# Kernel optimization log

Measured on AMD Instinct MI355X. Metric: run time of the kernel, lower is better.

## Reference

```python
import jax, jax.numpy as jnp
import numpy as np

N = 100000
E = 2000000
IN_DIM = 5
D = 32
L = 3
EPS = 1e-5


def setup_inputs() -> dict:
    key = jax.random.key(0)
    ks = jax.random.split(key, 10)
    x = jax.random.normal(ks[0], (N, IN_DIM), dtype=jnp.float32)
    edge_index = jax.random.randint(ks[1], (2, E), 0, N, dtype=jnp.int64)
    s = 1.0 / np.sqrt(D)
    w_in = jax.random.normal(ks[2], (D, IN_DIM), dtype=jnp.float32) / np.sqrt(IN_DIM)
    b_in = jnp.zeros((D,), dtype=jnp.float32)
    w_l = jax.random.normal(ks[3], (L, D, D), dtype=jnp.float32) * s  # lin_l per layer
    b_l = jnp.zeros((L, D), dtype=jnp.float32)
    w_r = jax.random.normal(ks[4], (L, D, D), dtype=jnp.float32) * s  # lin_r per layer (no bias, as in PyG SAGEConv)
    gamma = jnp.ones((D,), dtype=jnp.float32)
    beta = jnp.zeros((D,), dtype=jnp.float32)
    return {"x": x, "edge_index": edge_index, "w_in": w_in, "b_in": b_in,
            "w_l": w_l, "b_l": b_l, "w_r": w_r, "gamma": gamma, "beta": beta}


def _layernorm(h, gamma, beta):
    mu = jnp.mean(h, axis=-1, keepdims=True)
    var = jnp.mean(jnp.square(h - mu), axis=-1, keepdims=True)
    return (h - mu) * jax.lax.rsqrt(var + EPS) * gamma + beta


def reference(x, edge_index, w_in, b_in, w_l, b_l, w_r, gamma, beta):
    src = edge_index[0]
    dst = edge_index[1]
    n = x.shape[0]
    # node in-degree for mean aggregation (0-degree nodes get 0 output, like scatter_mean)
    deg = jax.ops.segment_sum(jnp.ones((src.shape[0],), dtype=x.dtype), dst, num_segments=n)
    inv_deg = (1.0 / jnp.maximum(deg, 1.0))[:, None]  # [N,1]
    h = x @ w_in.T + b_in  # [N, D]
    for i in range(w_l.shape[0]):
        msg = h[src]  # [E, D] gather
        agg = jax.ops.segment_sum(msg, dst, num_segments=n) * inv_deg  # mean aggregate
        h = agg @ w_l[i].T + b_l[i] + h @ w_r[i].T  # SAGEConv: lin_l(aggr) + lin_r(x)
        h = _layernorm(jax.nn.relu(h), gamma, beta)
    return h
```

## Files before the change

kernel.cpp:

```cpp
#include <hip/hip_runtime.h>
#include <hip/hip_bf16.h>

#define DIM 32
#define INDIM 5
#define EPB 4096
#define NBMAX 512
#define CAP 8192

__device__ __forceinline__ unsigned short f2bf(float f) {
    unsigned u = __float_as_uint(f);
    u += 0x7FFFu + ((u >> 16) & 1u);
    return (unsigned short)(u >> 16);
}
__device__ __forceinline__ float bf2f_lo(unsigned u) { return __uint_as_float(u << 16); }
__device__ __forceinline__ float bf2f_hi(unsigned u) { return __uint_as_float(u & 0xFFFF0000u); }


__global__ __launch_bounds__(256) void bucket_count_kernel(const int* __restrict__ dst,
                                                           int* __restrict__ bcnt, int e, int nb) {
    __shared__ int hist[NBMAX];
    int t = threadIdx.x;
    for (int i = t; i < nb; i += 256) hist[i] = 0;
    __syncthreads();
    int base = blockIdx.x * EPB;
    for (int k = 0; k < EPB; k += 256) {
        int i = base + k + t;
        if (i < e) atomicAdd(&hist[dst[i] >> 8], 1);
    }
    __syncthreads();
    for (int i = t; i < nb; i += 256) {
        int h = hist[i];
        if (h) atomicAdd(&bcnt[i], h);
    }
}


__global__ void bucket_scan_kernel(const int* __restrict__ bcnt, int* __restrict__ bbase,
                                   int* __restrict__ bcur, int* __restrict__ row_ptr,
                                   int nb, int n, int e) {
    __shared__ int s[512];
    int t = threadIdx.x;
    int v = (t < nb) ? bcnt[t] : 0;
    s[t] = v;
    __syncthreads();
    for (int o = 1; o < 512; o <<= 1) {
        int a = (t >= o) ? s[t - o] : 0;
        __syncthreads();
        s[t] += a;
        __syncthreads();
    }
    if (t < nb) {
        int excl = s[t] - v;
        bbase[t] = excl;
        bcur[t] = excl;
    }
    if (t == 0) {
        bbase[nb] = e;
        row_ptr[n] = e;
    }
}


__global__ __launch_bounds__(256) void bucket_fill_kernel(const int* __restrict__ src,
                                                          const int* __restrict__ dst,
                                                          int* __restrict__ bcur,
                                                          unsigned* __restrict__ packed,
                                                          int e, int nb) {
    __shared__ unsigned sw[EPB];
    __shared__ unsigned short sb[EPB];
    __shared__ int hist[NBMAX];
    __shared__ int rbase[NBMAX];
    int t = threadIdx.x;
    for (int i = t; i < nb; i += 256) hist[i] = 0;
    __syncthreads();
    int base = blockIdx.x * EPB;
    for (int k = 0; k < EPB; k += 256) {
        int i = base + k + t;
        if (i < e) {
            int s = src[i];
            int d = dst[i];
            int b = d >> 8;
            sw[k + t] = ((unsigned)s << 8) | (unsigned)(d & 255);
            sb[k + t] = (unsigned short)b;
            atomicAdd(&hist[b], 1);
        }
    }
    __syncthreads();
    for (int i = t; i < nb; i += 256) {
        int h = hist[i];
        rbase[i] = h ? atomicAdd(&bcur[i], h) : 0;
        hist[i] = 0;
    }
    __syncthreads();
    for (int k = 0; k < EPB; k += 256) {
        int i = base + k + t;
        if (i < e) {
            int b = sb[k + t];
            int r = atomicAdd(&hist[b], 1);
            packed[rbase[b] + r] = sw[k + t];
        }
    }
}


__global__ __launch_bounds__(256) void csr_build_kernel(const unsigned* __restrict__ packed,
                                                        const int* __restrict__ bbase,
                                                        int* __restrict__ row_ptr,
                                                        int* __restrict__ esrc, int n) {
    __shared__ unsigned ew[CAP];
    __shared__ int h2[256];
    __shared__ int off[256];
    int b = blockIdx.x;
    int base = bbase[b];
    int cnt = bbase[b + 1] - base;
    int t = threadIdx.x;
    h2[t] = 0;
    __syncthreads();
    bool staged = (cnt <= CAP);
    for (int i = t; i < cnt; i += 256) {
        unsigned w = packed[base + i];
        if (staged) ew[i] = w;
        atomicAdd(&h2[w & 255], 1);
    }
    __syncthreads();
    int v = h2[t];
    off[t] = v;
    __syncthreads();
    for (int o = 1; o < 256; o <<= 1) {
        int a = (t >= o) ? off[t - o] : 0;
        __syncthreads();
        off[t] += a;
        __syncthreads();
    }
    int excl = off[t] - v;
    __syncthreads();
    off[t] = excl;
    h2[t] = 0;
    __syncthreads();
    int node = b * 256 + t;
    if (node < n) row_ptr[node] = base + excl;
    for (int i = t; i < cnt; i += 256) {
        unsigned w = staged ? ew[i] : packed[base + i];
        int dl = w & 255;
        int r = atomicAdd(&h2[dl], 1);
        esrc[base + off[dl] + r] = (int)(w >> 8);
    }
}


__global__ void input_proj_kernel(const float* __restrict__ x, const float* __restrict__ w_in,
                                  const float* __restrict__ b_in,
                                  unsigned short* __restrict__ h, int n) {
    __shared__ float sw[DIM * INDIM];
    __shared__ float sb[DIM];
    int t = threadIdx.x;
    if (t < DIM * INDIM) sw[t] = w_in[t];
    if (t < DIM) sb[t] = b_in[t];
    __syncthreads();
    int idx = blockIdx.x * 256 + t;
    int node = idx >> 5;
    int d = idx & 31;
    if (node < n) {
        const float* xr = x + (size_t)node * INDIM;
        float acc = sb[d];
#pragma unroll
        for (int k = 0; k < INDIM; k++) acc = fmaf(xr[k], sw[d * INDIM + k], acc);
        h[(size_t)node * DIM + d] = f2bf(acc);
    }
}


template <int LAST>
__global__ __launch_bounds__(256, 4) void layer_fused_kernel(
    const int* __restrict__ row_ptr, const int* __restrict__ esrc,
    const unsigned short* __restrict__ h_in,
    unsigned short* __restrict__ h_out_bf, float* __restrict__ out_f32,
    const float* __restrict__ wl, const float* __restrict__ bl,
    const float* __restrict__ wr, const float* __restrict__ gamma,
    const float* __restrict__ beta, int n) {
    __shared__ float sAgg[64][DIM];
    __shared__ float sSelf[64][DIM];

    int t = threadIdx.x;
    int d = t & 31;

    float wlr[DIM], wrr[DIM];
    {
        const float4* p1 = (const float4*)(wl + (size_t)d * DIM);
        const float4* p2 = (const float4*)(wr + (size_t)d * DIM);
#pragma unroll
        for (int qq = 0; qq < 8; qq++) {
            float4 a = p1[qq];
            wlr[4 * qq] = a.x; wlr[4 * qq + 1] = a.y; wlr[4 * qq + 2] = a.z; wlr[4 * qq + 3] = a.w;
            float4 c = p2[qq];
            wrr[4 * qq] = c.x; wrr[4 * qq + 1] = c.y; wrr[4 * qq + 2] = c.z; wrr[4 * qq + 3] = c.w;
        }
    }
    float bias = bl[d], g = gamma[d], be = beta[d];

    int nd = t >> 2;
    int q = t & 3;
    int node = blockIdx.x * 64 + nd;
    const uint4* hv = (const uint4*)h_in;

    if (node < n) {
        {
            uint4 v = hv[(size_t)node * 4 + q];
            float4 f0 = make_float4(bf2f_lo(v.x), bf2f_hi(v.x), bf2f_lo(v.y), bf2f_hi(v.y));
            float4 f1 = make_float4(bf2f_lo(v.z), bf2f_hi(v.z), bf2f_lo(v.w), bf2f_hi(v.w));
            *(float4*)&sSelf[nd][q * 8] = f0;
            *(float4*)&sSelf[nd][q * 8 + 4] = f1;
        }
        int rs = row_ptr[node];
        int re = row_ptr[node + 1];
        float a0 = 0.f, a1 = 0.f, a2 = 0.f, a3 = 0.f, a4 = 0.f, a5 = 0.f, a6 = 0.f, a7 = 0.f;
        int j = rs;
        for (; j + 8 <= re; j += 8) {
            int s0 = esrc[j], s1 = esrc[j + 1], s2 = esrc[j + 2], s3 = esrc[j + 3];
            int s4 = esrc[j + 4], s5 = esrc[j + 5], s6 = esrc[j + 6], s7 = esrc[j + 7];
            uint4 v0 = hv[(size_t)s0 * 4 + q];
            uint4 v1 = hv[(size_t)s1 * 4 + q];
            uint4 v2 = hv[(size_t)s2 * 4 + q];
            uint4 v3 = hv[(size_t)s3 * 4 + q];
            uint4 v4 = hv[(size_t)s4 * 4 + q];
            uint4 v5 = hv[(size_t)s5 * 4 + q];
            uint4 v6 = hv[(size_t)s6 * 4 + q];
            uint4 v7 = hv[(size_t)s7 * 4 + q];
            a0 += bf2f_lo(v0.x); a1 += bf2f_hi(v0.x); a2 += bf2f_lo(v0.y); a3 += bf2f_hi(v0.y);
            a4 += bf2f_lo(v0.z); a5 += bf2f_hi(v0.z); a6 += bf2f_lo(v0.w); a7 += bf2f_hi(v0.w);
            a0 += bf2f_lo(v1.x); a1 += bf2f_hi(v1.x); a2 += bf2f_lo(v1.y); a3 += bf2f_hi(v1.y);
            a4 += bf2f_lo(v1.z); a5 += bf2f_hi(v1.z); a6 += bf2f_lo(v1.w); a7 += bf2f_hi(v1.w);
            a0 += bf2f_lo(v2.x); a1 += bf2f_hi(v2.x); a2 += bf2f_lo(v2.y); a3 += bf2f_hi(v2.y);
            a4 += bf2f_lo(v2.z); a5 += bf2f_hi(v2.z); a6 += bf2f_lo(v2.w); a7 += bf2f_hi(v2.w);
            a0 += bf2f_lo(v3.x); a1 += bf2f_hi(v3.x); a2 += bf2f_lo(v3.y); a3 += bf2f_hi(v3.y);
            a4 += bf2f_lo(v3.z); a5 += bf2f_hi(v3.z); a6 += bf2f_lo(v3.w); a7 += bf2f_hi(v3.w);
            a0 += bf2f_lo(v4.x); a1 += bf2f_hi(v4.x); a2 += bf2f_lo(v4.y); a3 += bf2f_hi(v4.y);
            a4 += bf2f_lo(v4.z); a5 += bf2f_hi(v4.z); a6 += bf2f_lo(v4.w); a7 += bf2f_hi(v4.w);
            a0 += bf2f_lo(v5.x); a1 += bf2f_hi(v5.x); a2 += bf2f_lo(v5.y); a3 += bf2f_hi(v5.y);
            a4 += bf2f_lo(v5.z); a5 += bf2f_hi(v5.z); a6 += bf2f_lo(v5.w); a7 += bf2f_hi(v5.w);
            a0 += bf2f_lo(v6.x); a1 += bf2f_hi(v6.x); a2 += bf2f_lo(v6.y); a3 += bf2f_hi(v6.y);
            a4 += bf2f_lo(v6.z); a5 += bf2f_hi(v6.z); a6 += bf2f_lo(v6.w); a7 += bf2f_hi(v6.w);
            a0 += bf2f_lo(v7.x); a1 += bf2f_hi(v7.x); a2 += bf2f_lo(v7.y); a3 += bf2f_hi(v7.y);
            a4 += bf2f_lo(v7.z); a5 += bf2f_hi(v7.z); a6 += bf2f_lo(v7.w); a7 += bf2f_hi(v7.w);
        }
        for (; j < re; ++j) {
            int s = esrc[j];
            uint4 v = hv[(size_t)s * 4 + q];
            a0 += bf2f_lo(v.x); a1 += bf2f_hi(v.x); a2 += bf2f_lo(v.y); a3 += bf2f_hi(v.y);
            a4 += bf2f_lo(v.z); a5 += bf2f_hi(v.z); a6 += bf2f_lo(v.w); a7 += bf2f_hi(v.w);
        }
        float iv = 1.f / fmaxf((float)(re - rs), 1.f);
        float4 f0 = make_float4(a0 * iv, a1 * iv, a2 * iv, a3 * iv);
        float4 f1 = make_float4(a4 * iv, a5 * iv, a6 * iv, a7 * iv);
        *(float4*)&sAgg[nd][q * 8] = f0;
        *(float4*)&sAgg[nd][q * 8 + 4] = f1;
    }
    __syncthreads();

#pragma unroll
    for (int it = 0; it < 8; ++it) {
        int ln = it * 8 + (t >> 5);
        int nodec = blockIdx.x * 64 + ln;
        if (nodec < n) {
            float o = bias;
            const float* va = sAgg[ln];
            const float* vs = sSelf[ln];
#pragma unroll
            for (int qq = 0; qq < 8; qq++) {
                float4 a = *(const float4*)&va[qq * 4];
                float4 s = *(const float4*)&vs[qq * 4];
                o = fmaf(a.x, wlr[4 * qq], o);     o = fmaf(s.x, wrr[4 * qq], o);
                o = fmaf(a.y, wlr[4 * qq + 1], o); o = fmaf(s.y, wrr[4 * qq + 1], o);
                o = fmaf(a.z, wlr[4 * qq + 2], o); o = fmaf(s.z, wrr[4 * qq + 2], o);
                o = fmaf(a.w, wlr[4 * qq + 3], o); o = fmaf(s.w, wrr[4 * qq + 3], o);
            }
            float out = fmaxf(o, 0.f);
            float sum = out, sq = out * out;
#pragma unroll
            for (int off = 16; off > 0; off >>= 1) {
                sum += __shfl_xor(sum, off, 32);
                sq += __shfl_xor(sq, off, 32);
            }
            float mu = sum * (1.f / 32.f);
            float var = fmaxf(sq * (1.f / 32.f) - mu * mu, 0.f);
            float r = rsqrtf(var + 1e-5f);
            float res = (out - mu) * r * g + be;
            if (LAST) out_f32[(size_t)nodec * DIM + d] = res;
            else      h_out_bf[(size_t)nodec * DIM + d] = f2bf(res);
        }
    }
}


extern "C" void kernel_launch(void* const* d_in, const int* in_sizes, int n_in,
                              void* d_out, int out_size, void* d_ws, size_t ws_size,
                              hipStream_t stream) {
    const float* x = (const float*)d_in[0];
    const int* ei = (const int*)d_in[1];
    const float* w_in = (const float*)d_in[2];
    const float* b_in = (const float*)d_in[3];
    const float* w_l = (const float*)d_in[4];
    const float* b_l = (const float*)d_in[5];
    const float* w_r = (const float*)d_in[6];
    const float* gamma = (const float*)d_in[7];
    const float* beta = (const float*)d_in[8];

    int n = in_sizes[0] / INDIM;
    int e = in_sizes[1] / 2;
    int L = in_sizes[4] / (DIM * DIM);
    const int* src = ei;
    const int* dst = ei + e;
    int nb = (n + 255) >> 8;

    char* w = (char*)d_ws;
    int* bcnt = (int*)w;               w += (size_t)NBMAX * 4;
    int* bbase = (int*)w;              w += (size_t)(NBMAX + 1) * 4;
    int* bcur = (int*)w;               w += (size_t)NBMAX * 4;
    int* row_ptr = (int*)w;            w += (size_t)(n + 1) * 4;
    int* esrc = (int*)w;               w += (size_t)e * 4;
    unsigned short* h_A = (unsigned short*)w;  w += (size_t)n * DIM * 2;
    unsigned short* h_B = (unsigned short*)w;  w += (size_t)n * DIM * 2;
    unsigned* packed = (unsigned*)h_A;

    int nbE = (e + EPB - 1) / EPB;

    hipMemsetAsync(bcnt, 0, (size_t)nb * 4, stream);
    bucket_count_kernel<<<nbE, 256, 0, stream>>>(dst, bcnt, e, nb);
    bucket_scan_kernel<<<1, 512, 0, stream>>>(bcnt, bbase, bcur, row_ptr, nb, n, e);
    bucket_fill_kernel<<<nbE, 256, 0, stream>>>(src, dst, bcur, packed, e, nb);
    csr_build_kernel<<<nb, 256, 0, stream>>>(packed, bbase, row_ptr, esrc, n);

    input_proj_kernel<<<(n * DIM + 255) / 256, 256, 0, stream>>>(x, w_in, b_in, h_A, n);

    unsigned short* bufs[2] = {h_A, h_B};
    int nbF = (n + 63) / 64;
    for (int i = 0; i < L; i++) {
        const unsigned short* hin = bufs[i & 1];
        unsigned short* hout = bufs[(i + 1) & 1];
        const float* wl = w_l + (size_t)i * DIM * DIM;
        const float* bl = b_l + (size_t)i * DIM;
        const float* wr = w_r + (size_t)i * DIM * DIM;
        if (i == L - 1)
            layer_fused_kernel<1><<<nbF, 256, 0, stream>>>(row_ptr, esrc, hin, nullptr,
                                                           (float*)d_out, wl, bl, wr,
                                                           gamma, beta, n);
        else
            layer_fused_kernel<0><<<nbF, 256, 0, stream>>>(row_ptr, esrc, hin, hout,
                                                           nullptr, wl, bl, wr,
                                                           gamma, beta, n);
    }
}
```

Measured before the change: 252.1 us.

## Shrink CSR buckets and layer blocks, prefetch edge indices, defer weight loads

CSR construction now uses 128-node buckets instead of 256, which doubles the number of csr_build blocks and halves the staging buffer. The fused layer kernel moves to 128-thread blocks covering 32 nodes each. It loads the next group of eight edge indices while the current group of gathers is in flight. It also loads the per-thread weight rows only after the aggregation phase, so those 64 registers are not held during the gather. The goals are higher occupancy and more memory-level parallelism in the latency-bound gather. The cost is more blocks, extra index registers, and a __syncthreads placed inside divergent branches in the bucket scan, which is fragile.

Measured after the change: 242.2 us. -3.9%, faster.

```diff
diff --git a/kernel.cpp b/kernel.cpp
--- a/kernel.cpp
+++ b/kernel.cpp
@@ -4,8 +4,10 @@
 #define DIM 32
 #define INDIM 5
 #define EPB 4096
-#define NBMAX 512
-#define CAP 8192
+#define BKBITS 7
+#define BKN 128
+#define NBMAX 1024
+#define CAP 4096
 
 __device__ __forceinline__ unsigned short f2bf(float f) {
     unsigned u = __float_as_uint(f);
@@ -25,7 +27,7 @@
     int base = blockIdx.x * EPB;
     for (int k = 0; k < EPB; k += 256) {
         int i = base + k + t;
-        if (i < e) atomicAdd(&hist[dst[i] >> 8], 1);
+        if (i < e) atomicAdd(&hist[dst[i] >> BKBITS], 1);
     }
     __syncthreads();
     for (int i = t; i < nb; i += 256) {
@@ -38,12 +40,12 @@
 __global__ void bucket_scan_kernel(const int* __restrict__ bcnt, int* __restrict__ bbase,
                                    int* __restrict__ bcur, int* __restrict__ row_ptr,
                                    int nb, int n, int e) {
-    __shared__ int s[512];
+    __shared__ int s[1024];
     int t = threadIdx.x;
     int v = (t < nb) ? bcnt[t] : 0;
     s[t] = v;
     __syncthreads();
-    for (int o = 1; o < 512; o <<= 1) {
+    for (int o = 1; o < 1024; o <<= 1) {
         int a = (t >= o) ? s[t - o] : 0;
         __syncthreads();
         s[t] += a;
@@ -79,8 +81,8 @@
         if (i < e) {
             int s = src[i];
             int d = dst[i];
-            int b = d >> 8;
-            sw[k + t] = ((unsigned)s << 8) | (unsigned)(d & 255);
+            int b = d >> BKBITS;
+            sw[k + t] = ((unsigned)s << BKBITS) | (unsigned)(d & (BKN - 1));
             sb[k + t] = (unsigned short)b;
             atomicAdd(&hist[b], 1);
         }
@@ -108,42 +110,50 @@
                                                         int* __restrict__ row_ptr,
                                                         int* __restrict__ esrc, int n) {
     __shared__ unsigned ew[CAP];
-    __shared__ int h2[256];
-    __shared__ int off[256];
+    __shared__ int h2[BKN];
+    __shared__ int off[BKN];
     int b = blockIdx.x;
     int base = bbase[b];
     int cnt = bbase[b + 1] - base;
     int t = threadIdx.x;
-    h2[t] = 0;
+    if (t < BKN) h2[t] = 0;
     __syncthreads();
     bool staged = (cnt <= CAP);
     for (int i = t; i < cnt; i += 256) {
         unsigned w = packed[base + i];
         if (staged) ew[i] = w;
-        atomicAdd(&h2[w & 255], 1);
-    }
-    __syncthreads();
-    int v = h2[t];
-    off[t] = v;
-    __syncthreads();
-    for (int o = 1; o < 256; o <<= 1) {
-        int a = (t >= o) ? off[t - o] : 0;
-        __syncthreads();
-        off[t] += a;
-        __syncthreads();
-    }
-    int excl = off[t] - v;
-    __syncthreads();
-    off[t] = excl;
-    h2[t] = 0;
-    __syncthreads();
-    int node = b * 256 + t;
-    if (node < n) row_ptr[node] = base + excl;
+        atomicAdd(&h2[w & (BKN - 1)], 1);
+    }
+    __syncthreads();
+    int v = 0;
+    if (t < BKN) {
+        v = h2[t];
+        off[t] = v;
+    }
+    __syncthreads();
+    for (int o = 1; o < BKN; o <<= 1) {
+        int a = 0;
+        if (t < BKN && t >= o) a = off[t - o];
+        __syncthreads();
+        if (t < BKN) off[t] += a;
+        __syncthreads();
+    }
+    if (t < BKN) {
+        int excl = off[t] - v;
+        __syncthreads();
+        off[t] = excl;
+        h2[t] = 0;
+    } else {
+        __syncthreads();
+    }
+    __syncthreads();
+    int node = b * BKN + t;
+    if (t < BKN && node < n) row_ptr[node] = base + off[t];
     for (int i = t; i < cnt; i += 256) {
         unsigned w = staged ? ew[i] : packed[base + i];
-        int dl = w & 255;
+        int dl = w & (BKN - 1);
         int r = atomicAdd(&h2[dl], 1);
-        esrc[base + off[dl] + r] = (int)(w >> 8);
+        esrc[base + off[dl] + r] = (int)(w >> BKBITS);
     }
 }
 
@@ -171,36 +181,22 @@
 
 
 template <int LAST>
-__global__ __launch_bounds__(256, 4) void layer_fused_kernel(
+__global__ __launch_bounds__(128, 4) void layer_fused_kernel(
     const int* __restrict__ row_ptr, const int* __restrict__ esrc,
     const unsigned short* __restrict__ h_in,
     unsigned short* __restrict__ h_out_bf, float* __restrict__ out_f32,
     const float* __restrict__ wl, const float* __restrict__ bl,
     const float* __restrict__ wr, const float* __restrict__ gamma,
     const float* __restrict__ beta, int n) {
-    __shared__ float sAgg[64][DIM];
-    __shared__ float sSelf[64][DIM];
+    __shared__ float sAgg[32][DIM];
+    __shared__ float sSelf[32][DIM];
 
     int t = threadIdx.x;
     int d = t & 31;
-
-    float wlr[DIM], wrr[DIM];
-    {
-        const float4* p1 = (const float4*)(wl + (size_t)d * DIM);
-        const float4* p2 = (const float4*)(wr + (size_t)d * DIM);
-#pragma unroll
-        for (int qq = 0; qq < 8; qq++) {
-            float4 a = p1[qq];
-            wlr[4 * qq] = a.x; wlr[4 * qq + 1] = a.y; wlr[4 * qq + 2] = a.z; wlr[4 * qq + 3] = a.w;
-            float4 c = p2[qq];
-            wrr[4 * qq] = c.x; wrr[4 * qq + 1] = c.y; wrr[4 * qq + 2] = c.z; wrr[4 * qq + 3] = c.w;
-        }
-    }
-    float bias = bl[d], g = gamma[d], be = beta[d];
 
     int nd = t >> 2;
     int q = t & 3;
-    int node = blockIdx.x * 64 + nd;
+    int node = blockIdx.x * 32 + nd;
     const uint4* hv = (const uint4*)h_in;
 
     if (node < n) {
@@ -215,17 +211,28 @@
         int re = row_ptr[node + 1];
         float a0 = 0.f, a1 = 0.f, a2 = 0.f, a3 = 0.f, a4 = 0.f, a5 = 0.f, a6 = 0.f, a7 = 0.f;
         int j = rs;
-        for (; j + 8 <= re; j += 8) {
-            int s0 = esrc[j], s1 = esrc[j + 1], s2 = esrc[j + 2], s3 = esrc[j + 3];
-            int s4 = esrc[j + 4], s5 = esrc[j + 5], s6 = esrc[j + 6], s7 = esrc[j + 7];
-            uint4 v0 = hv[(size_t)s0 * 4 + q];
-            uint4 v1 = hv[(size_t)s1 * 4 + q];
-            uint4 v2 = hv[(size_t)s2 * 4 + q];
-            uint4 v3 = hv[(size_t)s3 * 4 + q];
-            uint4 v4 = hv[(size_t)s4 * 4 + q];
-            uint4 v5 = hv[(size_t)s5 * 4 + q];
-            uint4 v6 = hv[(size_t)s6 * 4 + q];
-            uint4 v7 = hv[(size_t)s7 * 4 + q];
+        int i0, i1, i2, i3, i4, i5, i6, i7;
+        bool have = (j + 8 <= re);
+        if (have) {
+            i0 = esrc[j];     i1 = esrc[j + 1]; i2 = esrc[j + 2]; i3 = esrc[j + 3];
+            i4 = esrc[j + 4]; i5 = esrc[j + 5]; i6 = esrc[j + 6]; i7 = esrc[j + 7];
+        }
+        while (have) {
+            int jn = j + 8;
+            bool haven = (jn + 8 <= re);
+            int t0, t1, t2, t3, t4, t5, t6, t7;
+            if (haven) {
+                t0 = esrc[jn];     t1 = esrc[jn + 1]; t2 = esrc[jn + 2]; t3 = esrc[jn + 3];
+                t4 = esrc[jn + 4]; t5 = esrc[jn + 5]; t6 = esrc[jn + 6]; t7 = esrc[jn + 7];
+            }
+            uint4 v0 = hv[(size_t)i0 * 4 + q];
+            uint4 v1 = hv[(size_t)i1 * 4 + q];
+            uint4 v2 = hv[(size_t)i2 * 4 + q];
+            uint4 v3 = hv[(size_t)i3 * 4 + q];
+            uint4 v4 = hv[(size_t)i4 * 4 + q];
+            uint4 v5 = hv[(size_t)i5 * 4 + q];
+            uint4 v6 = hv[(size_t)i6 * 4 + q];
+            uint4 v7 = hv[(size_t)i7 * 4 + q];
             a0 += bf2f_lo(v0.x); a1 += bf2f_hi(v0.x); a2 += bf2f_lo(v0.y); a3 += bf2f_hi(v0.y);
             a4 += bf2f_lo(v0.z); a5 += bf2f_hi(v0.z); a6 += bf2f_lo(v0.w); a7 += bf2f_hi(v0.w);
             a0 += bf2f_lo(v1.x); a1 += bf2f_hi(v1.x); a2 += bf2f_lo(v1.y); a3 += bf2f_hi(v1.y);
@@ -242,6 +249,11 @@
             a4 += bf2f_lo(v6.z); a5 += bf2f_hi(v6.z); a6 += bf2f_lo(v6.w); a7 += bf2f_hi(v6.w);
             a0 += bf2f_lo(v7.x); a1 += bf2f_hi(v7.x); a2 += bf2f_lo(v7.y); a3 += bf2f_hi(v7.y);
             a4 += bf2f_lo(v7.z); a5 += bf2f_hi(v7.z); a6 += bf2f_lo(v7.w); a7 += bf2f_hi(v7.w);
+            j = jn;
+            have = haven;
+            if (haven) {
+                i0 = t0; i1 = t1; i2 = t2; i3 = t3; i4 = t4; i5 = t5; i6 = t6; i7 = t7;
+            }
         }
         for (; j < re; ++j) {
             int s = esrc[j];
@@ -257,10 +269,24 @@
     }
     __syncthreads();
 
+    float wlr[DIM], wrr[DIM];
+    {
+        const float4* p1 = (const float4*)(wl + (size_t)d * DIM);
+        const float4* p2 = (const float4*)(wr + (size_t)d * DIM);
+#pragma unroll
+        for (int qq = 0; qq < 8; qq++) {
+            float4 a = p1[qq];
+            wlr[4 * qq] = a.x; wlr[4 * qq + 1] = a.y; wlr[4 * qq + 2] = a.z; wlr[4 * qq + 3] = a.w;
+            float4 c = p2[qq];
+            wrr[4 * qq] = c.x; wrr[4 * qq + 1] = c.y; wrr[4 * qq + 2] = c.z; wrr[4 * qq + 3] = c.w;
+        }
+    }
+    float bias = bl[d], g = gamma[d], be = beta[d];
+
 #pragma unroll
     for (int it = 0; it < 8; ++it) {
-        int ln = it * 8 + (t >> 5);
-        int nodec = blockIdx.x * 64 + ln;
+        int ln = it * 4 + (t >> 5);
+        int nodec = blockIdx.x * 32 + ln;
         if (nodec < n) {
             float o = bias;
             const float* va = sAgg[ln];
@@ -310,7 +336,7 @@
     int L = in_sizes[4] / (DIM * DIM);
     const int* src = ei;
     const int* dst = ei + e;
-    int nb = (n + 255) >> 8;
+    int nb = (n + BKN - 1) >> BKBITS;
 
     char* w = (char*)d_ws;
     int* bcnt = (int*)w;               w += (size_t)NBMAX * 4;
@@ -326,14 +352,14 @@
 
     hipMemsetAsync(bcnt, 0, (size_t)nb * 4, stream);
     bucket_count_kernel<<<nbE, 256, 0, stream>>>(dst, bcnt, e, nb);
-    bucket_scan_kernel<<<1, 512, 0, stream>>>(bcnt, bbase, bcur, row_ptr, nb, n, e);
+    bucket_scan_kernel<<<1, 1024, 0, stream>>>(bcnt, bbase, bcur, row_ptr, nb, n, e);
     bucket_fill_kernel<<<nbE, 256, 0, stream>>>(src, dst, bcur, packed, e, nb);
     csr_build_kernel<<<nb, 256, 0, stream>>>(packed, bbase, row_ptr, esrc, n);
 
     input_proj_kernel<<<(n * DIM + 255) / 256, 256, 0, stream>>>(x, w_in, b_in, h_A, n);
 
     unsigned short* bufs[2] = {h_A, h_B};
-    int nbF = (n + 63) / 64;
+    int nbF = (n + 31) / 32;
     for (int i = 0; i < L; i++) {
         const unsigned short* hin = bufs[i & 1];
         unsigned short* hout = bufs[(i + 1) & 1];
@@ -341,11 +367,11 @@
         const float* bl = b_l + (size_t)i * DIM;
         const float* wr = w_r + (size_t)i * DIM * DIM;
         if (i == L - 1)
-            layer_fused_kernel<1><<<nbF, 256, 0, stream>>>(row_ptr, esrc, hin, nullptr,
+            layer_fused_kernel<1><<<nbF, 128, 0, stream>>>(row_ptr, esrc, hin, nullptr,
                                                            (float*)d_out, wl, bl, wr,
                                                            gamma, beta, n);
         else
-            layer_fused_kernel<0><<<nbF, 256, 0, stream>>>(row_ptr, esrc, hin, hout,
+            layer_fused_kernel<0><<<nbF, 128, 0, stream>>>(row_ptr, esrc, hin, hout,
                                                            nullptr, wl, bl, wr,
                                                            gamma, beta, n);
     }
```
